# Kernel optimization log

Measured on AMD Instinct MI355X. Metric: run time of the kernel, lower is better.

Reference implementation:

```python
import jax, jax.numpy as jnp
import numpy as np

B, S, H = 2, 2048, 2048
NH, NKV, HD = 16, 4, 128  # heads, kv heads, head_dim
GROUP = NH // NKV
THETA = 10000.0
NEG = -1e9


def _rope_tables(seq_len, head_dim, theta):
    inv_freq = 1.0 / (theta ** (jnp.arange(0, head_dim, 2, dtype=jnp.float32) / head_dim))
    t = jnp.arange(seq_len, dtype=jnp.float32)
    freqs = jnp.outer(t, inv_freq)                 # [S, HD/2]
    emb = jnp.concatenate([freqs, freqs], axis=-1)  # [S, HD]
    return jnp.cos(emb), jnp.sin(emb)


def _rotate_half(x):
    half = x.shape[-1] // 2
    return jnp.concatenate([-x[..., half:], x[..., :half]], axis=-1)


def setup_inputs() -> dict:
    key = jax.random.key(0)
    ks = jax.random.split(key, 5)
    scale = 0.02
    x = jax.random.normal(ks[0], (B, S, H), dtype=jnp.float32)
    Wq = jax.random.normal(ks[1], (NH * HD, H), dtype=jnp.float32) * scale
    Wk = jax.random.normal(ks[2], (NKV * HD, H), dtype=jnp.float32) * scale
    Wv = jax.random.normal(ks[3], (NKV * HD, H), dtype=jnp.float32) * scale
    Wo = jax.random.normal(ks[4], (H, NH * HD), dtype=jnp.float32) * scale
    cos, sin = _rope_tables(S, HD, THETA)
    # additive causal mask: 0 on/below diagonal, -1e9 above
    causal = jnp.triu(jnp.full((S, S), NEG, dtype=jnp.float32), k=1)
    mask = causal[None, None]  # [1,1,S,S]
    return {"x": x, "Wq": Wq, "Wk": Wk, "Wv": Wv, "Wo": Wo,
            "cos": cos, "sin": sin, "mask": mask}


def reference(x, Wq, Wk, Wv, Wo, cos, sin, mask):
    b, s, _ = x.shape
    # projections (nn.Linear, no bias): y = x @ W.T
    q = (x @ Wq.T).reshape(b, s, NH, HD).transpose(0, 2, 1, 3)    # [B,NH,S,D]
    k = (x @ Wk.T).reshape(b, s, NKV, HD).transpose(0, 2, 1, 3)   # [B,NKV,S,D]
    v = (x @ Wv.T).reshape(b, s, NKV, HD).transpose(0, 2, 1, 3)   # [B,NKV,S,D]
    # RoPE
    c = cos[None, None]  # [1,1,S,D]
    sn = sin[None, None]
    q = q * c + _rotate_half(q) * sn
    k = k * c + _rotate_half(k) * sn
    # GQA: repeat KV heads to match query heads (mirrors _repeat_kv)
    k = jnp.repeat(k, GROUP, axis=1)  # [B,NH,S,D]
    v = jnp.repeat(v, GROUP, axis=1)
    # scaled dot-product attention with additive mask
    scores = jnp.einsum('bhqd,bhkd->bhqk', q, k) / jnp.sqrt(jnp.float32(HD))
    scores = scores + mask
    p = jax.nn.softmax(scores, axis=-1)
    ctx = jnp.einsum('bhqk,bhkd->bhqd', p, v)            # [B,NH,S,D]
    ctx = ctx.transpose(0, 2, 1, 3).reshape(b, s, NH * HD)
    return ctx @ Wo.T
```

## Files before the change

kernel.cpp:

```cpp
#include <hip/hip_runtime.h>
#include <stdint.h>

#define B_   2
#define S_   2048
#define H_   2048
#define NH_  16
#define NKV_ 4
#define HD_  128
#define M_   (B_ * S_)

typedef short bf16x8 __attribute__((ext_vector_type(8)));
typedef float f32x4  __attribute__((ext_vector_type(4)));
typedef float f32x16 __attribute__((ext_vector_type(16)));

__device__ __forceinline__ float b2f(unsigned short u) {
  union { unsigned int u; float f; } v; v.u = ((unsigned int)u) << 16; return v.f;
}
__device__ __forceinline__ unsigned short f2b(float f) {
  union { float f; unsigned int u; } v; v.f = f;
  unsigned int u = v.u;
  unsigned int r = (u + 0x7FFFu + ((u >> 16) & 1u)) >> 16;
  return (unsigned short)r;
}
__device__ __forceinline__ uint4 pack8(const float4& a, const float4& b) {
  uint4 r;
  r.x = (unsigned)f2b(a.x) | ((unsigned)f2b(a.y) << 16);
  r.y = (unsigned)f2b(a.z) | ((unsigned)f2b(a.w) << 16);
  r.z = (unsigned)f2b(b.x) | ((unsigned)f2b(b.y) << 16);
  r.w = (unsigned)f2b(b.z) | ((unsigned)f2b(b.w) << 16);
  return r;
}
__device__ __forceinline__ void gload_lds(const unsigned short* g, unsigned short* l) {
  __builtin_amdgcn_global_load_lds(
      (const __attribute__((address_space(1))) unsigned int*)g,
      (__attribute__((address_space(3))) unsigned int*)l, 16, 0, 0);
}

__global__ void cvt_all(const float* __restrict__ x,  unsigned short* __restrict__ xb,
                        const float* __restrict__ wq, unsigned short* __restrict__ wqb,
                        const float* __restrict__ wk, unsigned short* __restrict__ wkb,
                        const float* __restrict__ wv, unsigned short* __restrict__ wvb,
                        const float* __restrict__ wo, unsigned short* __restrict__ wob)
{
  const int n8x = (M_ * H_) / 8;
  const int n8q = (H_ * H_) / 8;
  const int n8k = (NKV_ * HD_ * H_) / 8;
  int i = blockIdx.x * blockDim.x + threadIdx.x;
  const float* s; unsigned short* d; int off;
  if (i < n8x)                         { s = x;  d = xb;  off = i; }
  else if (i < n8x + n8q)              { s = wq; d = wqb; off = i - n8x; }
  else if (i < n8x + n8q + n8k)        { s = wk; d = wkb; off = i - n8x - n8q; }
  else if (i < n8x + n8q + 2 * n8k)    { s = wv; d = wvb; off = i - n8x - n8q - n8k; }
  else if (i < n8x + 2 * n8q + 2 * n8k){ s = wo; d = wob; off = i - n8x - n8q - 2 * n8k; }
  else return;
  const float* p = s + (size_t)off * 8;
  uint4 v = pack8(*reinterpret_cast<const float4*>(p), *reinterpret_cast<const float4*>(p + 4));
  *reinterpret_cast<uint4*>(d + (size_t)off * 8) = v;
}

__global__ __launch_bounds__(256, 4) void gemm_qkv(
    const unsigned short* __restrict__ A, const unsigned short* __restrict__ Wq,
    const unsigned short* __restrict__ Wk, const unsigned short* __restrict__ Wv,
    unsigned short* __restrict__ Qo, unsigned short* __restrict__ Ko,
    unsigned short* __restrict__ Vo)
{
  __shared__ unsigned short As[128 * 64];
  __shared__ unsigned short Bs[128 * 64];

  const int K = H_;
  const unsigned short* Bm; unsigned short* Cm; int colBase, N;
  const int bx = blockIdx.x;
  if (bx < 16)      { Bm = Wq; Cm = Qo; colBase = bx * 128;        N = NH_ * HD_;  }
  else if (bx < 20) { Bm = Wk; Cm = Ko; colBase = (bx - 16) * 128; N = NKV_ * HD_; }
  else              { Bm = Wv; Cm = Vo; colBase = (bx - 20) * 128; N = NKV_ * HD_; }
  const int rowBase = blockIdx.y * 128;

  const int tid    = threadIdx.x;
  const int lane   = tid & 63;
  const int wid    = tid >> 6;
  const int wrow   = wid >> 1;
  const int wcol   = wid & 1;
  const int lane15 = lane & 15;
  const int quad   = lane >> 4;

  const f32x4 zero = {0.f, 0.f, 0.f, 0.f};
  f32x4 acc[4][4];
#pragma unroll
  for (int i = 0; i < 4; i++)
#pragma unroll
    for (int j = 0; j < 4; j++) acc[i][j] = zero;

  const int lr  = lane >> 3;
  const int sc8 = (lane & 7) ^ lr;

  for (int kb = 0; kb < K; kb += 64) {
    __syncthreads();
#pragma unroll
    for (int i = 0; i < 4; i++) {
      const int rg = (i * 4 + wid) * 8;
      const int r  = rg + lr;
      gload_lds(A  + (size_t)(rowBase + r) * K + kb + sc8 * 8, As + rg * 64);
      gload_lds(Bm + (size_t)(colBase + r) * K + kb + sc8 * 8, Bs + rg * 64);
    }
    __syncthreads();
#pragma unroll
    for (int kc = 0; kc < 2; kc++) {
      bf16x8 af[4], bf[4];
#pragma unroll
      for (int g = 0; g < 4; g++) {
        const int ra = wrow * 64 + g * 16 + lane15;
        const int rb = wcol * 64 + g * 16 + lane15;
        af[g] = *reinterpret_cast<const bf16x8*>(As + ra * 64 + (((kc * 4 + quad) ^ (ra & 7)) * 8));
        bf[g] = *reinterpret_cast<const bf16x8*>(Bs + rb * 64 + (((kc * 4 + quad) ^ (rb & 7)) * 8));
      }
#pragma unroll
      for (int i = 0; i < 4; i++)
#pragma unroll
        for (int j = 0; j < 4; j++)
          acc[i][j] = __builtin_amdgcn_mfma_f32_16x16x32_bf16(af[i], bf[j], acc[i][j], 0, 0, 0);
    }
  }

#pragma unroll
  for (int i = 0; i < 4; i++) {
    int row = rowBase + wrow * 64 + i * 16 + quad * 4;
#pragma unroll
    for (int j = 0; j < 4; j++) {
      int col = colBase + wcol * 64 + j * 16 + lane15;
#pragma unroll
      for (int rr = 0; rr < 4; rr++)
        Cm[(size_t)(row + rr) * N + col] = f2b(acc[i][j][rr]);
    }
  }
}

template<bool CF32>
__global__ __launch_bounds__(256, 4) void gemm_ld(
    const unsigned short* __restrict__ A, const unsigned short* __restrict__ B0,
    const unsigned short* __restrict__ B1, void* __restrict__ C0, void* __restrict__ C1,
    int N, int K, int nxHalf)
{
  __shared__ unsigned short As[128 * 64];
  __shared__ unsigned short Bs[128 * 64];

  const unsigned short* Bm; void* Cm; int colBase;
  if ((int)blockIdx.x < nxHalf) { Bm = B0; Cm = C0; colBase = blockIdx.x * 128; }
  else                          { Bm = B1; Cm = C1; colBase = (blockIdx.x - nxHalf) * 128; }
  const int rowBase = blockIdx.y * 128;

  const int tid    = threadIdx.x;
  const int lane   = tid & 63;
  const int wid    = tid >> 6;
  const int wrow   = wid >> 1;
  const int wcol   = wid & 1;
  const int lane15 = lane & 15;
  const int quad   = lane >> 4;

  const f32x4 zero = {0.f, 0.f, 0.f, 0.f};
  f32x4 acc[4][4];
#pragma unroll
  for (int i = 0; i < 4; i++)
#pragma unroll
    for (int j = 0; j < 4; j++) acc[i][j] = zero;

  const int lr  = lane >> 3;
  const int sc8 = (lane & 7) ^ lr;

  for (int kb = 0; kb < K; kb += 64) {
    __syncthreads();
#pragma unroll
    for (int i = 0; i < 4; i++) {
      const int rg = (i * 4 + wid) * 8;
      const int r  = rg + lr;
      gload_lds(A  + (size_t)(rowBase + r) * K + kb + sc8 * 8, As + rg * 64);
      gload_lds(Bm + (size_t)(colBase + r) * K + kb + sc8 * 8, Bs + rg * 64);
    }
    __syncthreads();
#pragma unroll
    for (int kc = 0; kc < 2; kc++) {
      bf16x8 af[4], bf[4];
#pragma unroll
      for (int g = 0; g < 4; g++) {
        const int ra = wrow * 64 + g * 16 + lane15;
        const int rb = wcol * 64 + g * 16 + lane15;
        af[g] = *reinterpret_cast<const bf16x8*>(As + ra * 64 + (((kc * 4 + quad) ^ (ra & 7)) * 8));
        bf[g] = *reinterpret_cast<const bf16x8*>(Bs + rb * 64 + (((kc * 4 + quad) ^ (rb & 7)) * 8));
      }
#pragma unroll
      for (int i = 0; i < 4; i++)
#pragma unroll
        for (int j = 0; j < 4; j++)
          acc[i][j] = __builtin_amdgcn_mfma_f32_16x16x32_bf16(af[i], bf[j], acc[i][j], 0, 0, 0);
    }
  }

  if (CF32) {
    float* Cf = (float*)Cm;
#pragma unroll
    for (int i = 0; i < 4; i++) {
      int row = rowBase + wrow * 64 + i * 16 + quad * 4;
#pragma unroll
      for (int j = 0; j < 4; j++) {
        int col = colBase + wcol * 64 + j * 16 + lane15;
#pragma unroll
        for (int rr = 0; rr < 4; rr++)
          Cf[(size_t)(row + rr) * N + col] = acc[i][j][rr];
      }
    }
  } else {
    unsigned short* Cb = (unsigned short*)Cm;
#pragma unroll
    for (int i = 0; i < 4; i++) {
      int row = rowBase + wrow * 64 + i * 16 + quad * 4;
#pragma unroll
      for (int j = 0; j < 4; j++) {
        int col = colBase + wcol * 64 + j * 16 + lane15;
#pragma unroll
        for (int rr = 0; rr < 4; rr++)
          Cb[(size_t)(row + rr) * N + col] = f2b(acc[i][j][rr]);
      }
    }
  }
}

template<bool OPROJ>
__global__ __launch_bounds__(256, 3) void gemm_k(
    const void* __restrict__ A, const float* __restrict__ B0, const float* __restrict__ B1,
    void* __restrict__ C0, void* __restrict__ C1, int N, int K, int nxHalf)
{
  __shared__ unsigned short As[128 * 72];
  __shared__ unsigned short Bs[128 * 72];

  const float* Bm; void* Cm; int colBase;
  if ((int)blockIdx.x < nxHalf) { Bm = B0; Cm = C0; colBase = blockIdx.x * 128; }
  else                          { Bm = B1; Cm = C1; colBase = (blockIdx.x - nxHalf) * 128; }
  const int rowBase = blockIdx.y * 128;

  const int tid    = threadIdx.x;
  const int lane   = tid & 63;
  const int wid    = tid >> 6;
  const int wrow   = wid >> 1;
  const int wcol   = wid & 1;
  const int lane15 = lane & 15;
  const int quad   = lane >> 4;

  const f32x4 zero = {0.f, 0.f, 0.f, 0.f};
  f32x4 acc[4][4];
#pragma unroll
  for (int i = 0; i < 4; i++)
#pragma unroll
    for (int j = 0; j < 4; j++) acc[i][j] = zero;

  const int r0 = tid >> 3;
  const int c8 = tid & 7;

  uint4 av[4], bv[4];
#pragma unroll
  for (int p = 0; p < 4; p++) {
    int r = r0 + 32 * p;
    if (OPROJ) {
      av[p] = *reinterpret_cast<const uint4*>((const unsigned short*)A + (size_t)(rowBase + r) * K + c8 * 8);
    } else {
      const float* pA = (const float*)A + (size_t)(rowBase + r) * K + c8 * 8;
      av[p] = pack8(*reinterpret_cast<const float4*>(pA), *reinterpret_cast<const float4*>(pA + 4));
    }
    const float* pB = Bm + (size_t)(colBase + r) * K + c8 * 8;
    bv[p] = pack8(*reinterpret_cast<const float4*>(pB), *reinterpret_cast<const float4*>(pB + 4));
  }

  for (int kb = 0; kb < K; kb += 64) {
    __syncthreads();
#pragma unroll
    for (int p = 0; p < 4; p++) {
      int r = r0 + 32 * p;
      *reinterpret_cast<uint4*>(As + r * 72 + c8 * 8) = av[p];
      *reinterpret_cast<uint4*>(Bs + r * 72 + c8 * 8) = bv[p];
    }
    __syncthreads();
    const int kn = kb + 64;
    if (kn < K) {
#pragma unroll
      for (int p = 0; p < 4; p++) {
        int r = r0 + 32 * p;
        if (OPROJ) {
          av[p] = *reinterpret_cast<const uint4*>((const unsigned short*)A + (size_t)(rowBase + r) * K + kn + c8 * 8);
        } else {
          const float* pA = (const float*)A + (size_t)(rowBase + r) * K + kn + c8 * 8;
          av[p] = pack8(*reinterpret_cast<const float4*>(pA), *reinterpret_cast<const float4*>(pA + 4));
        }
        const float* pB = Bm + (size_t)(colBase + r) * K + kn + c8 * 8;
        bv[p] = pack8(*reinterpret_cast<const float4*>(pB), *reinterpret_cast<const float4*>(pB + 4));
      }
    }
#pragma unroll
    for (int kc = 0; kc < 2; kc++) {
      bf16x8 af[4], bf[4];
#pragma unroll
      for (int g = 0; g < 4; g++) {
        af[g] = *reinterpret_cast<const bf16x8*>(As + (wrow * 64 + g * 16 + lane15) * 72 + kc * 32 + quad * 8);
        bf[g] = *reinterpret_cast<const bf16x8*>(Bs + (wcol * 64 + g * 16 + lane15) * 72 + kc * 32 + quad * 8);
      }
#pragma unroll
      for (int i = 0; i < 4; i++)
#pragma unroll
        for (int j = 0; j < 4; j++)
          acc[i][j] = __builtin_amdgcn_mfma_f32_16x16x32_bf16(af[i], bf[j], acc[i][j], 0, 0, 0);
    }
  }

  if (OPROJ) {
    float* Cf = (float*)Cm;
#pragma unroll
    for (int i = 0; i < 4; i++) {
      int row = rowBase + wrow * 64 + i * 16 + quad * 4;
#pragma unroll
      for (int j = 0; j < 4; j++) {
        int col = colBase + wcol * 64 + j * 16 + lane15;
#pragma unroll
        for (int rr = 0; rr < 4; rr++)
          Cf[(size_t)(row + rr) * N + col] = acc[i][j][rr];
      }
    }
  } else {
    unsigned short* Cb = (unsigned short*)Cm;
#pragma unroll
    for (int i = 0; i < 4; i++) {
      int row = rowBase + wrow * 64 + i * 16 + quad * 4;
#pragma unroll
      for (int j = 0; j < 4; j++) {
        int col = colBase + wcol * 64 + j * 16 + lane15;
#pragma unroll
        for (int rr = 0; rr < 4; rr++)
          Cb[(size_t)(row + rr) * N + col] = f2b(acc[i][j][rr]);
      }
    }
  }
}

__global__ void rope_k(unsigned short* __restrict__ Qb, unsigned short* __restrict__ Kb,
                       const float* __restrict__ cosT, const float* __restrict__ sinT)
{
  const int per_tok = (NH_ + NKV_) * 64;
  int idx = blockIdx.x * blockDim.x + threadIdx.x;
  int t = idx / per_tok;
  int r = idx - t * per_tok;
  if (t >= M_) return;
  int s = t & (S_ - 1);
  unsigned short* base;
  int d;
  if (r < NH_ * 64) {
    int h = r >> 6; d = r & 63;
    base = Qb + (size_t)t * (NH_ * HD_) + h * HD_ + d;
  } else {
    int rk = r - NH_ * 64;
    int h = rk >> 6; d = rk & 63;
    base = Kb + (size_t)t * (NKV_ * HD_) + h * HD_ + d;
  }
  float c  = cosT[s * HD_ + d];
  float sn = sinT[s * HD_ + d];
  float x0 = b2f(base[0]);
  float x1 = b2f(base[64]);
  base[0]  = f2b(x0 * c - x1 * sn);
  base[64] = f2b(x1 * c + x0 * sn);
}

__global__ void transp_v(const unsigned short* __restrict__ Vb, unsigned short* __restrict__ VT)
{
  __shared__ unsigned short Ls[64 * 72];
  const int t0 = blockIdx.x * 64;
  const int d0 = blockIdx.y * 64;
  const int tid = threadIdx.x;
  const int r = tid >> 3, c = tid & 7;
#pragma unroll
  for (int p = 0; p < 2; p++)
    *reinterpret_cast<uint4*>(Ls + (r + 32 * p) * 72 + c * 8) =
      *reinterpret_cast<const uint4*>(Vb + (size_t)(t0 + r + 32 * p) * (NKV_ * HD_) + d0 + c * 8);
  __syncthreads();
  const int bq = t0 >> 11, s0 = t0 & (S_ - 1);
#pragma unroll
  for (int p = 0; p < 2; p++) {
    int dl = r + 32 * p;
    unsigned short tmp[8];
#pragma unroll
    for (int j = 0; j < 8; j++) tmp[j] = Ls[(c * 8 + j) * 72 + dl];
    *reinterpret_cast<uint4*>(VT + (size_t)(bq * 512 + d0 + dl) * S_ + s0 + c * 8) =
      *reinterpret_cast<uint4*>(tmp);
  }
}

__global__ __launch_bounds__(512, 1) void attn(
    const unsigned short* __restrict__ Q, const unsigned short* __restrict__ Kc,
    const unsigned short* __restrict__ VT, unsigned short* __restrict__ O)
{
  __shared__ unsigned short KsA[2 * 64 * 128];
  __shared__ unsigned short VsA[2 * 128 * 64];

  const int tid  = threadIdx.x;
  const int lane = tid & 63;
  const int w    = tid >> 6;
  const int l31  = lane & 31;
  const int hi   = lane >> 5;
  const int g    = blockIdx.x;
  const int kvh  = blockIdx.y;
  const int b    = blockIdx.z;
  const int h    = kvh * 4 + (w & 3);
  const int rg   = w >> 2;
  const size_t bS = (size_t)b * S_;
  const int nkt  = g + 1;
  const int qb   = g * 64;

  const int kr   = tid >> 4;
  const int kc16 = tid & 15;
  const int vd   = tid >> 3;
  const int vc8  = tid & 7;

  const unsigned short* Kbase = Kc + bS * (NKV_ * HD_) + kvh * HD_;
  const unsigned short* Vbase = VT + (size_t)(b * 512 + kvh * HD_) * S_;

  bf16x8 qf[8];
  {
    const unsigned short* qp = Q + (bS + qb + rg * 32 + l31) * (NH_ * HD_) + h * HD_ + hi * 8;
#pragma unroll
    for (int kc = 0; kc < 8; kc++) qf[kc] = *reinterpret_cast<const bf16x8*>(qp + kc * 16);
  }

  f32x16 ctx[4];
#pragma unroll
  for (int ng = 0; ng < 4; ng++)
#pragma unroll
    for (int r = 0; r < 16; r++) ctx[ng][r] = 0.f;
  float lsum = 0.f;

  const float scale = 0.08838834764831845f;

  uint4 kreg[2], vreg[2];
#pragma unroll
  for (int p2 = 0; p2 < 2; p2++) {
    kreg[p2] = *reinterpret_cast<const uint4*>(Kbase + (size_t)(kr + 32 * p2) * (NKV_ * HD_) + kc16 * 8);
    vreg[p2] = *reinterpret_cast<const uint4*>(Vbase + (size_t)(vd + 64 * p2) * S_ + vc8 * 8);
  }
#pragma unroll
  for (int p2 = 0; p2 < 2; p2++) {
    const int row = kr + 32 * p2;
    *reinterpret_cast<uint4*>(KsA + row * 128 + ((kc16 ^ (row & 15)) * 8)) = kreg[p2];
    const int d = vd + 64 * p2;
    *reinterpret_cast<uint4*>(VsA + d * 64 + ((vc8 ^ (d & 7)) * 8)) = vreg[p2];
  }
  __syncthreads();

  for (int kt = 0; kt < nkt; kt++) {
    unsigned short* ksc = KsA + (kt & 1) * 8192;
    unsigned short* vsc = VsA + (kt & 1) * 8192;
    unsigned short* ksn = KsA + ((kt & 1) ^ 1) * 8192;
    unsigned short* vsn = VsA + ((kt & 1) ^ 1) * 8192;

    if (kt + 1 < nkt) {
      const int key0 = (kt + 1) * 64;
#pragma unroll
      for (int p2 = 0; p2 < 2; p2++) {
        kreg[p2] = *reinterpret_cast<const uint4*>(Kbase + (size_t)(key0 + kr + 32 * p2) * (NKV_ * HD_) + kc16 * 8);
        vreg[p2] = *reinterpret_cast<const uint4*>(Vbase + (size_t)(vd + 64 * p2) * S_ + key0 + vc8 * 8);
      }
    }

    f32x16 sc0, sc1;
#pragma unroll
    for (int r = 0; r < 16; r++) { sc0[r] = 0.f; sc1[r] = 0.f; }
    __builtin_amdgcn_s_setprio(1);
#pragma unroll
    for (int kc = 0; kc < 8; kc++) {
      const int ch = ((kc * 2 + hi) ^ (l31 & 15)) * 8;
      bf16x8 kf0 = *reinterpret_cast<const bf16x8*>(ksc + l31 * 128 + ch);
      sc0 = __builtin_amdgcn_mfma_f32_32x32x16_bf16(kf0, qf[kc], sc0, 0, 0, 0);
      bf16x8 kf1 = *reinterpret_cast<const bf16x8*>(ksc + (32 + l31) * 128 + ch);
      sc1 = __builtin_amdgcn_mfma_f32_32x32x16_bf16(kf1, qf[kc], sc1, 0, 0, 0);
    }
    __builtin_amdgcn_s_setprio(0);

    const int lim = (kt == nkt - 1) ? (rg * 32 + l31) : 4096;
    bf16x8 pfrag[4];
#pragma unroll
    for (int cg = 0; cg < 2; cg++) {
      float pe[16];
#pragma unroll
      for (int r = 0; r < 16; r++) {
        float v = (cg ? sc1[r] : sc0[r]) * scale;
        const int kp = cg * 32 + (r & 3) + 8 * (r >> 2) + 4 * hi;
        v = (kp <= lim) ? v : -1.0e9f;
        float e = __expf(v);
        pe[r] = e;
        lsum += e;
      }
      unsigned wd[8];
#pragma unroll
      for (int j = 0; j < 8; j++) {
        unsigned t;
        asm("v_cvt_pk_bf16_f32 %0, %1, %2" : "=v"(t) : "v"(pe[2 * j]), "v"(pe[2 * j + 1]));
        wd[j] = t;
      }
      asm("v_permlane32_swap_b32 %0, %1" : "+v"(wd[0]), "+v"(wd[2]));
      asm("v_permlane32_swap_b32 %0, %1" : "+v"(wd[1]), "+v"(wd[3]));
      asm("v_permlane32_swap_b32 %0, %1" : "+v"(wd[4]), "+v"(wd[6]));
      asm("v_permlane32_swap_b32 %0, %1" : "+v"(wd[5]), "+v"(wd[7]));
      union { unsigned u[4]; bf16x8 v8; } ua, ub;
      ua.u[0] = wd[0]; ua.u[1] = wd[1]; ua.u[2] = wd[2]; ua.u[3] = wd[3];
      ub.u[0] = wd[4]; ub.u[1] = wd[5]; ub.u[2] = wd[6]; ub.u[3] = wd[7];
      pfrag[cg * 2]     = ua.v8;
      pfrag[cg * 2 + 1] = ub.v8;
    }

    __builtin_amdgcn_s_setprio(1);
#pragma unroll
    for (int ng = 0; ng < 4; ng++) {
      const int drow = ng * 32 + l31;
#pragma unroll
      for (int kc = 0; kc < 4; kc++) {
        bf16x8 vf = *reinterpret_cast<const bf16x8*>(vsc + drow * 64 + (((kc * 2 + hi) ^ (l31 & 7)) * 8));
        ctx[ng] = __builtin_amdgcn_mfma_f32_32x32x16_bf16(pfrag[kc], vf, ctx[ng], 0, 0, 0);
      }
    }
    __builtin_amdgcn_s_setprio(0);

    if (kt + 1 < nkt) {
#pragma unroll
      for (int p2 = 0; p2 < 2; p2++) {
        const int row = kr + 32 * p2;
        *reinterpret_cast<uint4*>(ksn + row * 128 + ((kc16 ^ (row & 15)) * 8)) = kreg[p2];
        const int d = vd + 64 * p2;
        *reinterpret_cast<uint4*>(vsn + d * 64 + ((vc8 ^ (d & 7)) * 8)) = vreg[p2];
      }
      __syncthreads();
    }
  }

  {
    float lt  = lsum + __shfl_xor(lsum, 32);
    float inv = 1.0f / lt;
    float il[16];
#pragma unroll
    for (int r = 0; r < 16; r++)
      il[r] = __shfl(inv, (r & 3) + 8 * (r >> 2) + 4 * hi);
    const size_t orow0 = bS + qb + rg * 32;
#pragma unroll
    for (int ng = 0; ng < 4; ng++)
#pragma unroll
      for (int r = 0; r < 16; r++) {
        const int qp = (r & 3) + 8 * (r >> 2) + 4 * hi;
        O[(orow0 + qp) * (NH_ * HD_) + h * HD_ + ng * 32 + l31] = f2b(ctx[ng][r] * il[r]);
      }
  }
}

extern "C" void kernel_launch(void* const* d_in, const int* in_sizes, int n_in,
                              void* d_out, int out_size, void* d_ws, size_t ws_size,
                              hipStream_t stream) {
  const float* x    = (const float*)d_in[0];
  const float* Wq   = (const float*)d_in[1];
  const float* Wk   = (const float*)d_in[2];
  const float* Wv   = (const float*)d_in[3];
  const float* Wo   = (const float*)d_in[4];
  const float* cosT = (const float*)d_in[5];
  const float* sinT = (const float*)d_in[6];
  float* out = (float*)d_out;

  const size_t qElems  = (size_t)M_ * NH_ * HD_;
  const size_t xElems  = (size_t)M_ * H_;
  const size_t wqElems = (size_t)H_ * H_;
  const size_t wkElems = (size_t)NKV_ * HD_ * H_;
  const size_t bigNeed = (qElems + xElems + 2 * wqElems + 2 * wkElems) * 2 + 256;

  if (ws_size < qElems * 2 + 256) return;

  unsigned short* Qb = (unsigned short*)d_ws;
  unsigned short* Kb = (unsigned short*)d_out;
  unsigned short* Vb = Kb + (size_t)M_ * NKV_ * HD_;
  unsigned short* VT = Vb + (size_t)M_ * NKV_ * HD_;

  dim3 blk(256);
  const int rope_threads = M_ * (NH_ + NKV_) * 64;

  if (ws_size >= bigNeed) {
    unsigned short* xb  = Qb + qElems;
    unsigned short* Wqb = xb + xElems;
    unsigned short* Wob = Wqb + wqElems;
    unsigned short* Wkb = Wob + wqElems;
    unsigned short* Wvb = Wkb + wkElems;

    const int n8tot = (int)((xElems + 2 * wqElems + 2 * wkElems) / 8);
    cvt_all<<<dim3((n8tot + 255) / 256), blk, 0, stream>>>(
        x, xb, Wq, Wqb, Wk, Wkb, Wv, Wvb, Wo, Wob);

    gemm_qkv<<<dim3(24, 32), blk, 0, stream>>>(xb, Wqb, Wkb, Wvb, Qb, Kb, Vb);

    rope_k<<<dim3((rope_threads + 255) / 256), blk, 0, stream>>>(Qb, Kb, cosT, sinT);
    transp_v<<<dim3(M_ / 64, (NKV_ * HD_) / 64), blk, 0, stream>>>(Vb, VT);
    attn<<<dim3(32, NKV_, B_), dim3(512), 0, stream>>>(Qb, Kb, VT, Qb);

    gemm_ld<true><<<dim3(16, 32), blk, 0, stream>>>(Qb, Wob, Wob, out, out, H_, NH_ * HD_, 16);
  } else {
    gemm_k<false><<<dim3(16, 32), blk, 0, stream>>>(x, Wq, Wq, Qb, Qb, NH_ * HD_, H_, 16);
    gemm_k<false><<<dim3(8, 32), blk, 0, stream>>>(x, Wk, Wv, Kb, Vb, NKV_ * HD_, H_, 4);

    rope_k<<<dim3((rope_threads + 255) / 256), blk, 0, stream>>>(Qb, Kb, cosT, sinT);
    transp_v<<<dim3(M_ / 64, (NKV_ * HD_) / 64), blk, 0, stream>>>(Vb, VT);
    attn<<<dim3(32, NKV_, B_), dim3(512), 0, stream>>>(Qb, Kb, VT, Qb);

    gemm_k<true><<<dim3(16, 32), blk, 0, stream>>>(Qb, Wo, Wo, out, out, H_, NH_ * HD_, 16);
  }
}
```

Before: 321.7 us.

## Pair causal query tiles per attention block to balance work

Each attention block now processes two query tiles, (31-p) and p, one after the other, so every block covers the same total number of key tiles under the causal mask. The block shrinks from 512 to 256 threads, each block covers two heads instead of four, and K/V loads per thread double to fill the same tiles. The aim is to remove the tail imbalance of the triangular causal workload. In exchange, K/V tiles are shared by fewer heads per block, so there is more redundant K/V traffic and fewer waves per block to hide latency.

```diff
diff --git a/kernel.cpp b/kernel.cpp
--- a/kernel.cpp
+++ b/kernel.cpp
@@ -388,7 +388,7 @@
   }
 }
 
-__global__ __launch_bounds__(512, 1) void attn(
+__global__ __launch_bounds__(256, 1) void attn(
     const unsigned short* __restrict__ Q, const unsigned short* __restrict__ Kc,
     const unsigned short* __restrict__ VT, unsigned short* __restrict__ O)
 {
@@ -400,14 +400,22 @@
   const int w    = tid >> 6;
   const int l31  = lane & 31;
   const int hi   = lane >> 5;
-  const int g    = blockIdx.x;
+  const int x    = blockIdx.x;
+  const int p    = x & 15;
+  const int hh   = x >> 4;
   const int kvh  = blockIdx.y;
   const int b    = blockIdx.z;
-  const int h    = kvh * 4 + (w & 3);
-  const int rg   = w >> 2;
+  const int h    = kvh * 4 + hh * 2 + (w & 1);
+  const int rg   = w >> 1;
   const size_t bS = (size_t)b * S_;
-  const int nkt  = g + 1;
-  const int qb   = g * 64;
+
+  const int qt1  = 31 - p;
+  const int qt2  = p;
+  const int nkt1 = qt1 + 1;
+  const int nkt2 = qt2 + 1;
+  const int ntot = nkt1 + nkt2;
+  const int qb1  = qt1 * 64;
+  const int qb2  = qt2 * 64;
 
   const int kr   = tid >> 4;
   const int kc16 = tid & 15;
@@ -419,7 +427,7 @@
 
   bf16x8 qf[8];
   {
-    const unsigned short* qp = Q + (bS + qb + rg * 32 + l31) * (NH_ * HD_) + h * HD_ + hi * 8;
+    const unsigned short* qp = Q + (bS + qb1 + rg * 32 + l31) * (NH_ * HD_) + h * HD_ + hi * 8;
 #pragma unroll
     for (int kc = 0; kc < 8; kc++) qf[kc] = *reinterpret_cast<const bf16x8*>(qp + kc * 16);
   }
@@ -433,33 +441,37 @@
 
   const float scale = 0.08838834764831845f;
 
-  uint4 kreg[2], vreg[2];
-#pragma unroll
-  for (int p2 = 0; p2 < 2; p2++) {
-    kreg[p2] = *reinterpret_cast<const uint4*>(Kbase + (size_t)(kr + 32 * p2) * (NKV_ * HD_) + kc16 * 8);
-    vreg[p2] = *reinterpret_cast<const uint4*>(Vbase + (size_t)(vd + 64 * p2) * S_ + vc8 * 8);
-  }
-#pragma unroll
-  for (int p2 = 0; p2 < 2; p2++) {
-    const int row = kr + 32 * p2;
+  uint4 kreg[4], vreg[4];
+#pragma unroll
+  for (int p2 = 0; p2 < 4; p2++) {
+    kreg[p2] = *reinterpret_cast<const uint4*>(Kbase + (size_t)(kr + 16 * p2) * (NKV_ * HD_) + kc16 * 8);
+    vreg[p2] = *reinterpret_cast<const uint4*>(Vbase + (size_t)(vd + 32 * p2) * S_ + vc8 * 8);
+  }
+#pragma unroll
+  for (int p2 = 0; p2 < 4; p2++) {
+    const int row = kr + 16 * p2;
     *reinterpret_cast<uint4*>(KsA + row * 128 + ((kc16 ^ (row & 15)) * 8)) = kreg[p2];
-    const int d = vd + 64 * p2;
+    const int d = vd + 32 * p2;
     *reinterpret_cast<uint4*>(VsA + d * 64 + ((vc8 ^ (d & 7)) * 8)) = vreg[p2];
   }
   __syncthreads();
 
-  for (int kt = 0; kt < nkt; kt++) {
-    unsigned short* ksc = KsA + (kt & 1) * 8192;
-    unsigned short* vsc = VsA + (kt & 1) * 8192;
-    unsigned short* ksn = KsA + ((kt & 1) ^ 1) * 8192;
-    unsigned short* vsn = VsA + ((kt & 1) ^ 1) * 8192;
-
-    if (kt + 1 < nkt) {
-      const int key0 = (kt + 1) * 64;
-#pragma unroll
-      for (int p2 = 0; p2 < 2; p2++) {
-        kreg[p2] = *reinterpret_cast<const uint4*>(Kbase + (size_t)(key0 + kr + 32 * p2) * (NKV_ * HD_) + kc16 * 8);
-        vreg[p2] = *reinterpret_cast<const uint4*>(Vbase + (size_t)(vd + 64 * p2) * S_ + key0 + vc8 * 8);
+  for (int seq = 0; seq < ntot; seq++) {
+    const bool ph1 = (seq < nkt1);
+    const int kt   = ph1 ? seq : seq - nkt1;
+    const int nkt  = ph1 ? nkt1 : nkt2;
+    unsigned short* ksc = KsA + (seq & 1) * 8192;
+    unsigned short* vsc = VsA + (seq & 1) * 8192;
+    unsigned short* ksn = KsA + ((seq & 1) ^ 1) * 8192;
+    unsigned short* vsn = VsA + ((seq & 1) ^ 1) * 8192;
+
+    if (seq + 1 < ntot) {
+      const int ktn  = (seq + 1 < nkt1) ? seq + 1 : seq + 1 - nkt1;
+      const int key0 = ktn * 64;
+#pragma unroll
+      for (int p2 = 0; p2 < 4; p2++) {
+        kreg[p2] = *reinterpret_cast<const uint4*>(Kbase + (size_t)(key0 + kr + 16 * p2) * (NKV_ * HD_) + kc16 * 8);
+        vreg[p2] = *reinterpret_cast<const uint4*>(Vbase + (size_t)(vd + 32 * p2) * S_ + key0 + vc8 * 8);
       }
     }
 
@@ -521,33 +533,44 @@
     }
     __builtin_amdgcn_s_setprio(0);
 
-    if (kt + 1 < nkt) {
-#pragma unroll
-      for (int p2 = 0; p2 < 2; p2++) {
-        const int row = kr + 32 * p2;
+    if (seq + 1 < ntot) {
+#pragma unroll
+      for (int p2 = 0; p2 < 4; p2++) {
+        const int row = kr + 16 * p2;
         *reinterpret_cast<uint4*>(ksn + row * 128 + ((kc16 ^ (row & 15)) * 8)) = kreg[p2];
-        const int d = vd + 64 * p2;
+        const int d = vd + 32 * p2;
         *reinterpret_cast<uint4*>(vsn + d * 64 + ((vc8 ^ (d & 7)) * 8)) = vreg[p2];
       }
-      __syncthreads();
-    }
-  }
-
-  {
-    float lt  = lsum + __shfl_xor(lsum, 32);
-    float inv = 1.0f / lt;
-    float il[16];
-#pragma unroll
-    for (int r = 0; r < 16; r++)
-      il[r] = __shfl(inv, (r & 3) + 8 * (r >> 2) + 4 * hi);
-    const size_t orow0 = bS + qb + rg * 32;
-#pragma unroll
-    for (int ng = 0; ng < 4; ng++)
-#pragma unroll
-      for (int r = 0; r < 16; r++) {
-        const int qp = (r & 3) + 8 * (r >> 2) + 4 * hi;
-        O[(orow0 + qp) * (NH_ * HD_) + h * HD_ + ng * 32 + l31] = f2b(ctx[ng][r] * il[r]);
-      }
+    }
+
+    if (kt == nkt - 1) {
+      float lt  = lsum + __shfl_xor(lsum, 32);
+      float inv = 1.0f / lt;
+      float il[16];
+#pragma unroll
+      for (int r = 0; r < 16; r++)
+        il[r] = __shfl(inv, (r & 3) + 8 * (r >> 2) + 4 * hi);
+      const size_t orow0 = bS + (ph1 ? qb1 : qb2) + rg * 32;
+#pragma unroll
+      for (int ng = 0; ng < 4; ng++)
+#pragma unroll
+        for (int r = 0; r < 16; r++) {
+          const int qp = (r & 3) + 8 * (r >> 2) + 4 * hi;
+          O[(orow0 + qp) * (NH_ * HD_) + h * HD_ + ng * 32 + l31] = f2b(ctx[ng][r] * il[r]);
+        }
+      if (ph1) {
+        const unsigned short* qp2 = Q + (bS + qb2 + rg * 32 + l31) * (NH_ * HD_) + h * HD_ + hi * 8;
+#pragma unroll
+        for (int kc = 0; kc < 8; kc++) qf[kc] = *reinterpret_cast<const bf16x8*>(qp2 + kc * 16);
+#pragma unroll
+        for (int ng = 0; ng < 4; ng++)
+#pragma unroll
+          for (int r = 0; r < 16; r++) ctx[ng][r] = 0.f;
+        lsum = 0.f;
+      }
+    }
+
+    if (seq + 1 < ntot) __syncthreads();
   }
 }
 
@@ -594,7 +617,7 @@
 
     rope_k<<<dim3((rope_threads + 255) / 256), blk, 0, stream>>>(Qb, Kb, cosT, sinT);
     transp_v<<<dim3(M_ / 64, (NKV_ * HD_) / 64), blk, 0, stream>>>(Vb, VT);
-    attn<<<dim3(32, NKV_, B_), dim3(512), 0, stream>>>(Qb, Kb, VT, Qb);
+    attn<<<dim3(32, NKV_, B_), dim3(256), 0, stream>>>(Qb, Kb, VT, Qb);
 
     gemm_ld<true><<<dim3(16, 32), blk, 0, stream>>>(Qb, Wob, Wob, out, out, H_, NH_ * HD_, 16);
   } else {
@@ -603,7 +626,7 @@
 
     rope_k<<<dim3((rope_threads + 255) / 256), blk, 0, stream>>>(Qb, Kb, cosT, sinT);
     transp_v<<<dim3(M_ / 64, (NKV_ * HD_) / 64), blk, 0, stream>>>(Vb, VT);
-    attn<<<dim3(32, NKV_, B_), dim3(512), 0, stream>>>(Qb, Kb, VT, Qb);
+    attn<<<dim3(32, NKV_, B_), dim3(256), 0, stream>>>(Qb, Kb, VT, Qb);
 
     gemm_k<true><<<dim3(16, 32), blk, 0, stream>>>(Qb, Wo, Wo, out, out, H_, NH_ * HD_, 16);
   }
```

After: 353.5 us. +9.9%, slower.
